# Kernel tuning notes

Measured on AMD Instinct MI355X. Metric: run time of the kernel, lower is better.

Reference implementation:

```python
import jax, jax.numpy as jnp
import numpy as np

NUM_NODES = 50000
NUM_EDGES = 640000
H_DIM = 128
OUT_DIM = 128
NUM_RELS = 16
NUM_BASES = 8


def _rgcn_layer(h, basis, coef, bias, src, dst, etype, norm, activation):
    # Basis decomposition: W[r] = sum_b coef[r,b] * basis[b]  -> [R, d_in, d_out]
    W = jnp.einsum('rb,bio->rio', coef, basis)
    # Transform node features under every relation: [R, N, d_out]
    Hr = jnp.einsum('ni,rio->rno', h, W)
    # Per-edge message: pick (relation, source) pair, apply edge norm. [E, d_out]
    msg = Hr[etype, src] * norm
    # Aggregate messages at destination nodes. [N, d_out]
    out = jax.ops.segment_sum(msg, dst, num_segments=h.shape[0])
    out = out + bias
    return activation(out) if activation is not None else out


def setup_inputs() -> dict:
    key = jax.random.key(0)
    ks = jax.random.split(key, 10)
    h = jax.random.normal(ks[0], (NUM_NODES, H_DIM), dtype=jnp.float32)
    norm = jax.random.uniform(ks[1], (NUM_EDGES, 1), dtype=jnp.float32)
    src = jax.random.randint(ks[2], (NUM_EDGES,), 0, NUM_NODES, dtype=jnp.int32)
    dst = jax.random.randint(ks[3], (NUM_EDGES,), 0, NUM_NODES, dtype=jnp.int32)
    etype = jax.random.randint(ks[4], (NUM_EDGES,), 0, NUM_RELS, dtype=jnp.int32)
    s1 = 1.0 / np.sqrt(H_DIM)
    s2 = 1.0 / np.sqrt(H_DIM)
    V1 = jax.random.normal(ks[5], (NUM_BASES, H_DIM, H_DIM), dtype=jnp.float32) * s1
    coef1 = jax.random.normal(ks[6], (NUM_RELS, NUM_BASES), dtype=jnp.float32) * (1.0 / np.sqrt(NUM_BASES))
    bias1 = jnp.zeros((H_DIM,), dtype=jnp.float32)
    V2 = jax.random.normal(ks[7], (NUM_BASES, H_DIM, OUT_DIM), dtype=jnp.float32) * s2
    coef2 = jax.random.normal(ks[8], (NUM_RELS, NUM_BASES), dtype=jnp.float32) * (1.0 / np.sqrt(NUM_BASES))
    bias2 = jnp.zeros((OUT_DIM,), dtype=jnp.float32)
    return {
        'h': h, 'norm': norm, 'src': src, 'dst': dst, 'etype': etype,
        'V1': V1, 'coef1': coef1, 'bias1': bias1,
        'V2': V2, 'coef2': coef2, 'bias2': bias2,
    }


def reference(h, norm, src, dst, etype, V1, coef1, bias1, V2, coef2, bias2):
    # Layer 0: relational graph conv with ReLU (hidden layer)
    h1 = _rgcn_layer(h, V1, coef1, bias1, src, dst, etype, norm, jax.nn.relu)
    # Layer 1+: BaseRGCN sorts edges by relation (bucketing for the low-mem
    # per-relation dispatch). The sort is a permutation of the edge set, so we
    # mirror it explicitly; the segment_sum result is mathematically identical.
    order = jnp.argsort(etype)
    src_s, dst_s, et_s, norm_s = src[order], dst[order], etype[order], norm[order]
    out = _rgcn_layer(h1, V2, coef2, bias2, src_s, dst_s, et_s, norm_s, None)
    return out
```

## Files before the change

### kernel.cpp

```cpp
#include <hip/hip_runtime.h>

#define N_RELS 16
#define N_BASES 8
#define HD 128
#define SCAN_B 1024
#define ROWS 32

typedef __attribute__((ext_vector_type(8))) short bf16x8;
typedef __attribute__((ext_vector_type(4))) float floatx4;
typedef __attribute__((ext_vector_type(2))) float floatx2;

__device__ __forceinline__ short bf16rn(float f) {
    union { float f; unsigned u; } v; v.f = f;
    unsigned u = v.u;
    unsigned r = (u + 0x7fffu + ((u >> 16) & 1u)) >> 16;
    return (short)r;
}

__device__ __forceinline__ unsigned packbf2(floatx2 a) {
    return ((unsigned)(unsigned short)bf16rn(a.y) << 16) | (unsigned short)bf16rn(a.x);
}


__global__ void setup_fused(const float* __restrict__ h, unsigned* __restrict__ hb, int n4,
                            const float* __restrict__ V1, const float* __restrict__ V2,
                            short* __restrict__ Vf,
                            const int* __restrict__ dst, int E, int* __restrict__ cnt,
                            int packBlocks, int vBlocks) {
    int blk = blockIdx.x;
    if (blk < packBlocks) {
        int i = blk * blockDim.x + threadIdx.x;
        if (i < n4) {
            float4 v = ((const float4*)h)[i];
            uint2 o;
            o.x = ((unsigned)(unsigned short)bf16rn(v.y) << 16) | (unsigned short)bf16rn(v.x);
            o.y = ((unsigned)(unsigned short)bf16rn(v.w) << 16) | (unsigned short)bf16rn(v.z);
            ((uint2*)hb)[i] = o;
        }
        return;
    }
    blk -= packBlocks;
    if (blk < vBlocks) {
        const float* V = ((blk & 8) ? V2 : V1) + (size_t)(blk & 7) * 16384;
        size_t obase = (size_t)blk * 16384;
        for (int e = threadIdx.x; e < 16384; e += blockDim.x) {
            float w = V[e];
            int k = e >> 7, n = e & 127;
            int kk = k >> 5, q = (k >> 3) & 3, j = k & 7;
            int lane = q * 16 + (n & 15);
            int idx = ((kk * 8 + (n >> 4)) * 64 + lane) * 8 + j;
            Vf[obase + idx] = bf16rn(w);
        }
        return;
    }
    blk -= vBlocks;
    int i = blk * blockDim.x + threadIdx.x;
    if (i < E) atomicAdd(&cnt[dst[i]], 1);
}


__global__ void scan_partial(const int* __restrict__ cnt, int N,
                             int* __restrict__ excl, int* __restrict__ bsum) {
    __shared__ int s[SCAN_B];
    int t = threadIdx.x, i = blockIdx.x * SCAN_B + t;
    int v = (i < N) ? cnt[i] : 0;
    s[t] = v; __syncthreads();
    for (int o = 1; o < SCAN_B; o <<= 1) {
        int x = (t >= o) ? s[t - o] : 0;
        __syncthreads();
        s[t] += x;
        __syncthreads();
    }
    if (i < N) excl[i] = s[t] - v;
    if (t == SCAN_B - 1) bsum[blockIdx.x] = s[t];
}

__global__ void scan_fixup(int* __restrict__ row_ptr, const int* __restrict__ bsum,
                           int nb, int N, int E, int* __restrict__ cursor) {
    __shared__ int pref[64];
    int t = threadIdx.x;
    if (t < 64) {
        int raw = (t < nb) ? bsum[t] : 0;
        int v = raw;
#pragma unroll
        for (int o = 1; o < 64; o <<= 1) {
            int u = __shfl_up(v, o, 64);
            if (t >= o) v += u;
        }
        pref[t] = v - raw;
    }
    __syncthreads();
    int i = blockIdx.x * blockDim.x + t;
    if (i < N) { int val = row_ptr[i] + pref[i >> 10]; row_ptr[i] = val; cursor[i] = val; }
    if (i == 0) row_ptr[N] = E;
}

__global__ void scatter_dst(const int* __restrict__ dst, const int* __restrict__ src,
                            const int* __restrict__ et, const float* __restrict__ norm,
                            int E, int* __restrict__ cursor, int2* __restrict__ edata) {
    int i = blockIdx.x * blockDim.x + threadIdx.x;
    if (i >= E) return;
    int p = atomicAdd(&cursor[dst[i]], 1);
    edata[p] = make_int2((et[i] << 16) | src[i], __float_as_int(norm[i]));
}


__global__ __launch_bounds__(512, 4) void rgcn_tile(
    const unsigned* __restrict__ hb, const int2* __restrict__ edata,
    const int* __restrict__ row_ptr, const float* __restrict__ coef,
    const short* __restrict__ Vf, const float* __restrict__ bias,
    void* __restrict__ outp, int N, int E, int mode) {
    __shared__ __align__(16) unsigned Zs[N_BASES][4][4][ROWS + 1][4];
    __shared__ __align__(16) float cofs[N_RELS * N_BASES];

    const int tid = threadIdx.x;
    const int wave = tid >> 6, lane = tid & 63;
    const int l16 = lane & 15;
    const int nb0 = blockIdx.x * ROWS;

    if (tid < N_RELS * N_BASES) cofs[tid] = coef[tid];
    __syncthreads();

    const int r = tid >> 4;
    const int node = nb0 + (r & 31);
    const int cn = (node < N) ? node : (N - 1);
    const int s = row_ptr[cn];
    const int t = row_ptr[cn + 1];
    const int len = (node < N) ? (t - s) : 0;

    int mx = len;
    mx = max(mx, __shfl_xor(mx, 16, 64));
    mx = max(mx, __shfl_xor(mx, 32, 64));
    const int nG = __builtin_amdgcn_readfirstlane(mx);

    floatx2 acc[4][N_BASES] = {};

    auto edix = [&](int j) { int ix = s + j; return (ix > E - 1) ? (E - 1) : ix; };
    auto gath = [&](int2 m) {
        return ((const uint4*)(hb + (size_t)(m.x & 0xffff) * 64))[l16];
    };
    auto procG = [&](int2 m, uint4 g, int j) {
        float nv = (j < len) ? __int_as_float(m.y) : 0.f;
        int ets = m.x >> 16;
        floatx4 c0 = *(const floatx4*)&cofs[ets * 8];
        floatx4 c1 = *(const floatx4*)&cofs[ets * 8 + 4];
        floatx2 v0, v1, v2, v3;
        v0.x = __uint_as_float(g.x << 16) * nv; v0.y = __uint_as_float(g.x & 0xffff0000u) * nv;
        v1.x = __uint_as_float(g.y << 16) * nv; v1.y = __uint_as_float(g.y & 0xffff0000u) * nv;
        v2.x = __uint_as_float(g.z << 16) * nv; v2.y = __uint_as_float(g.z & 0xffff0000u) * nv;
        v3.x = __uint_as_float(g.w << 16) * nv; v3.y = __uint_as_float(g.w & 0xffff0000u) * nv;
#pragma unroll
        for (int b = 0; b < N_BASES; b++) {
            float cw = (b < 4) ? c0[b & 3] : c1[b & 3];
            acc[0][b] = v0 * cw + acc[0][b];
            acc[1][b] = v1 * cw + acc[1][b];
            acc[2][b] = v2 * cw + acc[2][b];
            acc[3][b] = v3 * cw + acc[3][b];
        }
    };

    int2 m0 = edata[edix(0)];
    uint4 g0 = gath(m0);
    int2 m1 = edata[edix(1)];

    int k = 0;
    for (; k + 2 <= nG; k += 2) {
        uint4 g1 = gath(m1);
        procG(m0, g0, k);
        m0 = edata[edix(k + 2)];
        g0 = gath(m0);
        procG(m1, g1, k + 1);
        m1 = edata[edix(k + 3)];
    }
    if (k < nG) procG(m0, g0, k);

    {
        uint4 w;
#pragma unroll
        for (int b = 0; b < N_BASES; b++) {
            w.x = packbf2(acc[0][b]);
            w.y = packbf2(acc[1][b]);
            w.z = packbf2(acc[2][b]);
            w.w = packbf2(acc[3][b]);
            *(uint4*)&Zs[b][l16 >> 2][l16 & 3][r & 31][0] = w;
        }
    }
    __syncthreads();

    const int q = lane >> 4, cc = lane & 15;
    const int tt = wave;
    floatx4 ac0 = {}, ac1 = {};

#pragma unroll 2
    for (int b = 0; b < N_BASES; b++) {
#pragma unroll
        for (int kk = 0; kk < 4; kk++) {
            bf16x8 a0 = *(const bf16x8*)&Zs[b][kk][q][cc][0];
            bf16x8 a1 = *(const bf16x8*)&Zs[b][kk][q][16 + cc][0];
            bf16x8 B = *(const bf16x8*)(Vf + (size_t)b * 16384 +
                                        ((size_t)(kk * 8 + tt) * 64 + lane) * 8);
            ac0 = __builtin_amdgcn_mfma_f32_16x16x32_bf16(a0, B, ac0, 0, 0, 0);
            ac1 = __builtin_amdgcn_mfma_f32_16x16x32_bf16(a1, B, ac1, 0, 0, 0);
        }
    }

    float bv = bias[tt * 16 + cc];
    if (mode == 0) {
        unsigned short* o = (unsigned short*)outp;
#pragma unroll
        for (int mi = 0; mi < 2; mi++) {
            const floatx4& c = mi ? ac1 : ac0;
#pragma unroll
            for (int i = 0; i < 4; i++) {
                int nd = nb0 + mi * 16 + q * 4 + i;
                if (nd < N) {
                    float v = fmaxf(c[i] + bv, 0.f);
                    o[(size_t)nd * HD + tt * 16 + cc] = (unsigned short)bf16rn(v);
                }
            }
        }
    } else {
        float* o = (float*)outp;
#pragma unroll
        for (int mi = 0; mi < 2; mi++) {
            const floatx4& c = mi ? ac1 : ac0;
#pragma unroll
            for (int i = 0; i < 4; i++) {
                int nd = nb0 + mi * 16 + q * 4 + i;
                if (nd < N) o[(size_t)nd * HD + tt * 16 + cc] = c[i] + bv;
            }
        }
    }
}


extern "C" void kernel_launch(void* const* d_in, const int* in_sizes, int n_in,
                              void* d_out, int out_size, void* d_ws, size_t ws_size,
                              hipStream_t stream) {
    const float* h     = (const float*)d_in[0];
    const float* norm  = (const float*)d_in[1];
    const int*   src   = (const int*)d_in[2];
    const int*   dst   = (const int*)d_in[3];
    const int*   etype = (const int*)d_in[4];
    const float* V1    = (const float*)d_in[5];
    const float* coef1 = (const float*)d_in[6];
    const float* bias1 = (const float*)d_in[7];
    const float* V2    = (const float*)d_in[8];
    const float* coef2 = (const float*)d_in[9];
    const float* bias2 = (const float*)d_in[10];
    const int N = in_sizes[0] / HD;
    const int E = in_sizes[2];
    float* out = (float*)d_out;
    (void)n_in; (void)out_size; (void)ws_size;

    char* ws = (char*)d_ws;
    size_t off = 0;
    auto alloc = [&](size_t bytes) {
        void* p = ws + off;
        off += (bytes + 255) & ~(size_t)255;
        return p;
    };
    short*    Vf      = (short*)alloc((size_t)16 * 16384 * sizeof(short));
    unsigned* hb      = (unsigned*)alloc((size_t)N * 64 * sizeof(unsigned));
    unsigned* h1b     = (unsigned*)alloc((size_t)N * 64 * sizeof(unsigned));
    int2*     edata   = (int2*)alloc((size_t)E * sizeof(int2));
    int*      cnt     = (int*)alloc((size_t)N * sizeof(int));
    int*      row_ptr = (int*)alloc((size_t)(N + 1) * sizeof(int));
    int*      cursor  = (int*)alloc((size_t)N * sizeof(int));
    int*      bsum    = (int*)alloc(256 * sizeof(int));

    const int nb = (N + SCAN_B - 1) / SCAN_B;
    const int packBlocks = (N * 32 + 255) / 256;
    const int vBlocks = 16;
    const int histBlocks = (E + 255) / 256;

    hipMemsetAsync(cnt, 0, (size_t)N * sizeof(int), stream);
    setup_fused<<<packBlocks + vBlocks + histBlocks, 256, 0, stream>>>(
        h, hb, N * 32, V1, V2, Vf, dst, E, cnt, packBlocks, vBlocks);
    scan_partial<<<nb, SCAN_B, 0, stream>>>(cnt, N, row_ptr, bsum);
    scan_fixup<<<(N + 255) / 256, 256, 0, stream>>>(row_ptr, bsum, nb, N, E, cursor);
    scatter_dst<<<(E + 255) / 256, 256, 0, stream>>>(dst, src, etype, norm, E, cursor, edata);

    const int tiles = (N + ROWS - 1) / ROWS;

    rgcn_tile<<<tiles, 512, 0, stream>>>(hb, edata, row_ptr, coef1, Vf, bias1, h1b, N, E, 0);
    rgcn_tile<<<tiles, 512, 0, stream>>>(h1b, edata, row_ptr, coef2, Vf + (size_t)8 * 16384,
                                         bias2, out, N, E, 1);
}
```

Before: 304.6 us.

## Halve rows per block and spread each node's gather across 32 lanes

Each block now handles 16 destination nodes instead of 32. Each node gets 32 lanes that each load 4 bf16 features (uint2), where before 16 lanes each loaded 8. This halves per-thread accumulator registers and doubles the lanes per node, and the edge gather loop is deepened to a 3-way rotating pipeline unrolled by 6. The intent is more memory-level parallelism and occupancy for the irregular gather. In exchange it launches twice as many blocks, reloads the V basis per block for half as many rows, and wastes more iterations when nG is not a multiple of 6.

```diff
diff --git a/kernel.cpp b/kernel.cpp
--- a/kernel.cpp
+++ b/kernel.cpp
@@ -4,7 +4,7 @@
 #define N_BASES 8
 #define HD 128
 #define SCAN_B 1024
-#define ROWS 32
+#define ROWS 16
 
 typedef __attribute__((ext_vector_type(8))) short bf16x8;
 typedef __attribute__((ext_vector_type(4))) float floatx4;
@@ -115,92 +115,77 @@
 
     const int tid = threadIdx.x;
     const int wave = tid >> 6, lane = tid & 63;
-    const int l16 = lane & 15;
+    const int l32 = tid & 31;
     const int nb0 = blockIdx.x * ROWS;
 
     if (tid < N_RELS * N_BASES) cofs[tid] = coef[tid];
     __syncthreads();
 
-    const int r = tid >> 4;
-    const int node = nb0 + (r & 31);
+    const int r = tid >> 5;
+    const int node = nb0 + r;
     const int cn = (node < N) ? node : (N - 1);
     const int s = row_ptr[cn];
-    const int t = row_ptr[cn + 1];
-    const int len = (node < N) ? (t - s) : 0;
-
-    int mx = len;
-    mx = max(mx, __shfl_xor(mx, 16, 64));
-    mx = max(mx, __shfl_xor(mx, 32, 64));
+    const int len = (node < N) ? (row_ptr[cn + 1] - s) : 0;
+
+    int mx = max(len, __shfl_xor(len, 32, 64));
     const int nG = __builtin_amdgcn_readfirstlane(mx);
 
-    floatx2 acc[4][N_BASES] = {};
+    floatx2 a0[N_BASES] = {}, a1[N_BASES] = {};
+    const uint2* hbp = (const uint2*)hb;
 
     auto edix = [&](int j) { int ix = s + j; return (ix > E - 1) ? (E - 1) : ix; };
-    auto gath = [&](int2 m) {
-        return ((const uint4*)(hb + (size_t)(m.x & 0xffff) * 64))[l16];
-    };
-    auto procG = [&](int2 m, uint4 g, int j) {
+    auto gath = [&](int2 m) { return hbp[(size_t)(m.x & 0xffff) * 32 + l32]; };
+    auto proc = [&](int2 m, uint2 g, int j) {
         float nv = (j < len) ? __int_as_float(m.y) : 0.f;
         int ets = m.x >> 16;
         floatx4 c0 = *(const floatx4*)&cofs[ets * 8];
         floatx4 c1 = *(const floatx4*)&cofs[ets * 8 + 4];
-        floatx2 v0, v1, v2, v3;
+        floatx2 v0, v1;
         v0.x = __uint_as_float(g.x << 16) * nv; v0.y = __uint_as_float(g.x & 0xffff0000u) * nv;
         v1.x = __uint_as_float(g.y << 16) * nv; v1.y = __uint_as_float(g.y & 0xffff0000u) * nv;
-        v2.x = __uint_as_float(g.z << 16) * nv; v2.y = __uint_as_float(g.z & 0xffff0000u) * nv;
-        v3.x = __uint_as_float(g.w << 16) * nv; v3.y = __uint_as_float(g.w & 0xffff0000u) * nv;
 #pragma unroll
         for (int b = 0; b < N_BASES; b++) {
-            float cw = (b < 4) ? c0[b & 3] : c1[b & 3];
-            acc[0][b] = v0 * cw + acc[0][b];
-            acc[1][b] = v1 * cw + acc[1][b];
-            acc[2][b] = v2 * cw + acc[2][b];
-            acc[3][b] = v3 * cw + acc[3][b];
+            float cw = (b < 4) ? c0[b] : c1[b - 4];
+            a0[b] = v0 * cw + a0[b];
+            a1[b] = v1 * cw + a1[b];
         }
     };
 
-    int2 m0 = edata[edix(0)];
-    uint4 g0 = gath(m0);
-    int2 m1 = edata[edix(1)];
-
-    int k = 0;
-    for (; k + 2 <= nG; k += 2) {
-        uint4 g1 = gath(m1);
-        procG(m0, g0, k);
-        m0 = edata[edix(k + 2)];
-        g0 = gath(m0);
-        procG(m1, g1, k + 1);
-        m1 = edata[edix(k + 3)];
-    }
-    if (k < nG) procG(m0, g0, k);
+    int2 mA = edata[edix(0)], mB = edata[edix(1)], mC = edata[edix(2)];
+    uint2 gA = gath(mA), gB;
+
+    for (int k = 0; k < nG; k += 6) {
+        gB = gath(mB); proc(mA, gA, k);     mA = edata[edix(k + 3)];
+        gA = gath(mC); proc(mB, gB, k + 1); mB = edata[edix(k + 4)];
+        gB = gath(mA); proc(mC, gA, k + 2); mC = edata[edix(k + 5)];
+        gA = gath(mB); proc(mA, gB, k + 3); mA = edata[edix(k + 6)];
+        gB = gath(mC); proc(mB, gA, k + 4); mB = edata[edix(k + 7)];
+        gA = gath(mA); proc(mC, gB, k + 5); mC = edata[edix(k + 8)];
+    }
 
     {
-        uint4 w;
+        uint2 w;
 #pragma unroll
         for (int b = 0; b < N_BASES; b++) {
-            w.x = packbf2(acc[0][b]);
-            w.y = packbf2(acc[1][b]);
-            w.z = packbf2(acc[2][b]);
-            w.w = packbf2(acc[3][b]);
-            *(uint4*)&Zs[b][l16 >> 2][l16 & 3][r & 31][0] = w;
+            w.x = packbf2(a0[b]);
+            w.y = packbf2(a1[b]);
+            *(uint2*)&Zs[b][l32 >> 3][(l32 >> 1) & 3][r][(l32 & 1) * 2] = w;
         }
     }
     __syncthreads();
 
     const int q = lane >> 4, cc = lane & 15;
     const int tt = wave;
-    floatx4 ac0 = {}, ac1 = {};
+    floatx4 ac = {};
 
 #pragma unroll 2
     for (int b = 0; b < N_BASES; b++) {
 #pragma unroll
         for (int kk = 0; kk < 4; kk++) {
-            bf16x8 a0 = *(const bf16x8*)&Zs[b][kk][q][cc][0];
-            bf16x8 a1 = *(const bf16x8*)&Zs[b][kk][q][16 + cc][0];
+            bf16x8 a = *(const bf16x8*)&Zs[b][kk][q][cc][0];
             bf16x8 B = *(const bf16x8*)(Vf + (size_t)b * 16384 +
                                         ((size_t)(kk * 8 + tt) * 64 + lane) * 8);
-            ac0 = __builtin_amdgcn_mfma_f32_16x16x32_bf16(a0, B, ac0, 0, 0, 0);
-            ac1 = __builtin_amdgcn_mfma_f32_16x16x32_bf16(a1, B, ac1, 0, 0, 0);
+            ac = __builtin_amdgcn_mfma_f32_16x16x32_bf16(a, B, ac, 0, 0, 0);
         }
     }
 
@@ -208,27 +193,19 @@
     if (mode == 0) {
         unsigned short* o = (unsigned short*)outp;
 #pragma unroll
-        for (int mi = 0; mi < 2; mi++) {
-            const floatx4& c = mi ? ac1 : ac0;
-#pragma unroll
-            for (int i = 0; i < 4; i++) {
-                int nd = nb0 + mi * 16 + q * 4 + i;
-                if (nd < N) {
-                    float v = fmaxf(c[i] + bv, 0.f);
-                    o[(size_t)nd * HD + tt * 16 + cc] = (unsigned short)bf16rn(v);
-                }
+        for (int i = 0; i < 4; i++) {
+            int nd = nb0 + q * 4 + i;
+            if (nd < N) {
+                float v = fmaxf(ac[i] + bv, 0.f);
+                o[(size_t)nd * HD + tt * 16 + cc] = (unsigned short)bf16rn(v);
             }
         }
     } else {
         float* o = (float*)outp;
 #pragma unroll
-        for (int mi = 0; mi < 2; mi++) {
-            const floatx4& c = mi ? ac1 : ac0;
-#pragma unroll
-            for (int i = 0; i < 4; i++) {
-                int nd = nb0 + mi * 16 + q * 4 + i;
-                if (nd < N) o[(size_t)nd * HD + tt * 16 + cc] = c[i] + bv;
-            }
+        for (int i = 0; i < 4; i++) {
+            int nd = nb0 + q * 4 + i;
+            if (nd < N) o[(size_t)nd * HD + tt * 16 + cc] = ac[i] + bv;
         }
     }
 }
```

Result: slower. 355.5 us (+16.7%).

## Merge setup, histogram, scan and scatter into one cooperative kernel

Applied to the files above, without the earlier changes.

Replaces the memset and four preprocessing launches (pack/histogram, two scan passes, scatter) with a single cooperative kernel that uses grid-wide syncs between phases. The scan is redone as 64-element wave chunks with a single-wave pass over chunk sums. The goal is to remove launch overhead and inter-kernel gaps. In exchange it adds grid.sync barriers, fixes the grid at 1024 blocks, and serialises the chunk-sum scan on one wave, which could be slower than the separate kernels.

```diff
diff --git a/kernel.cpp b/kernel.cpp
--- a/kernel.cpp
+++ b/kernel.cpp
@@ -1,9 +1,11 @@
 #include <hip/hip_runtime.h>
+#include <hip/hip_cooperative_groups.h>
+
+namespace cg = cooperative_groups;
 
 #define N_RELS 16
 #define N_BASES 8
 #define HD 128
-#define SCAN_B 1024
 #define ROWS 32
 
 typedef __attribute__((ext_vector_type(8))) short bf16x8;
@@ -22,86 +24,93 @@
 }
 
 
-__global__ void setup_fused(const float* __restrict__ h, unsigned* __restrict__ hb, int n4,
-                            const float* __restrict__ V1, const float* __restrict__ V2,
-                            short* __restrict__ Vf,
-                            const int* __restrict__ dst, int E, int* __restrict__ cnt,
-                            int packBlocks, int vBlocks) {
-    int blk = blockIdx.x;
-    if (blk < packBlocks) {
-        int i = blk * blockDim.x + threadIdx.x;
-        if (i < n4) {
-            float4 v = ((const float4*)h)[i];
-            uint2 o;
-            o.x = ((unsigned)(unsigned short)bf16rn(v.y) << 16) | (unsigned short)bf16rn(v.x);
-            o.y = ((unsigned)(unsigned short)bf16rn(v.w) << 16) | (unsigned short)bf16rn(v.z);
-            ((uint2*)hb)[i] = o;
-        }
-        return;
-    }
-    blk -= packBlocks;
-    if (blk < vBlocks) {
+__global__ void setup_all(const float* __restrict__ h, unsigned* __restrict__ hb,
+                          const float* __restrict__ V1, const float* __restrict__ V2,
+                          short* __restrict__ Vf,
+                          const int* __restrict__ dst, const int* __restrict__ src,
+                          const int* __restrict__ et, const float* __restrict__ norm,
+                          int* __restrict__ cnt, int* __restrict__ row_ptr,
+                          int* __restrict__ cursor, int* __restrict__ bsum,
+                          int* __restrict__ bpre, int2* __restrict__ edata,
+                          int N, int E) {
+    cg::grid_group grid = cg::this_grid();
+    const int tid = threadIdx.x;
+    const int gid = blockIdx.x;
+    const int gtid = gid * blockDim.x + tid;
+    const int GSZ = gridDim.x * blockDim.x;
+    const int lane = tid & 63;
+    const int nchunk = (N + 63) >> 6;
+
+    for (int i = gtid; i < N; i += GSZ) cnt[i] = 0;
+    const int n4 = N * 32;
+    for (int i = gtid; i < n4; i += GSZ) {
+        float4 v = ((const float4*)h)[i];
+        uint2 o;
+        o.x = ((unsigned)(unsigned short)bf16rn(v.y) << 16) | (unsigned short)bf16rn(v.x);
+        o.y = ((unsigned)(unsigned short)bf16rn(v.w) << 16) | (unsigned short)bf16rn(v.z);
+        ((uint2*)hb)[i] = o;
+    }
+    for (int x = gtid; x < 16 * 16384; x += GSZ) {
+        int blk = x >> 14, e = x & 16383;
         const float* V = ((blk & 8) ? V2 : V1) + (size_t)(blk & 7) * 16384;
-        size_t obase = (size_t)blk * 16384;
-        for (int e = threadIdx.x; e < 16384; e += blockDim.x) {
-            float w = V[e];
-            int k = e >> 7, n = e & 127;
-            int kk = k >> 5, q = (k >> 3) & 3, j = k & 7;
-            int lane = q * 16 + (n & 15);
-            int idx = ((kk * 8 + (n >> 4)) * 64 + lane) * 8 + j;
-            Vf[obase + idx] = bf16rn(w);
-        }
-        return;
-    }
-    blk -= vBlocks;
-    int i = blk * blockDim.x + threadIdx.x;
-    if (i < E) atomicAdd(&cnt[dst[i]], 1);
-}
-
-
-__global__ void scan_partial(const int* __restrict__ cnt, int N,
-                             int* __restrict__ excl, int* __restrict__ bsum) {
-    __shared__ int s[SCAN_B];
-    int t = threadIdx.x, i = blockIdx.x * SCAN_B + t;
-    int v = (i < N) ? cnt[i] : 0;
-    s[t] = v; __syncthreads();
-    for (int o = 1; o < SCAN_B; o <<= 1) {
-        int x = (t >= o) ? s[t - o] : 0;
-        __syncthreads();
-        s[t] += x;
-        __syncthreads();
-    }
-    if (i < N) excl[i] = s[t] - v;
-    if (t == SCAN_B - 1) bsum[blockIdx.x] = s[t];
-}
-
-__global__ void scan_fixup(int* __restrict__ row_ptr, const int* __restrict__ bsum,
-                           int nb, int N, int E, int* __restrict__ cursor) {
-    __shared__ int pref[64];
-    int t = threadIdx.x;
-    if (t < 64) {
-        int raw = (t < nb) ? bsum[t] : 0;
-        int v = raw;
+        float w = V[e];
+        int k = e >> 7, n = e & 127;
+        int kk = k >> 5, q = (k >> 3) & 3, j = k & 7;
+        int ln = q * 16 + (n & 15);
+        int idx = ((kk * 8 + (n >> 4)) * 64 + ln) * 8 + j;
+        Vf[(size_t)blk * 16384 + idx] = bf16rn(w);
+    }
+    grid.sync();
+
+    for (int i = gtid; i < E; i += GSZ) atomicAdd(&cnt[dst[i]], 1);
+    grid.sync();
+
+    if (gid < nchunk && tid < 64) {
+        int i = gid * 64 + lane;
+        int v = (i < N) ? cnt[i] : 0;
+        int incl = v;
 #pragma unroll
         for (int o = 1; o < 64; o <<= 1) {
-            int u = __shfl_up(v, o, 64);
-            if (t >= o) v += u;
-        }
-        pref[t] = v - raw;
-    }
-    __syncthreads();
-    int i = blockIdx.x * blockDim.x + t;
-    if (i < N) { int val = row_ptr[i] + pref[i >> 10]; row_ptr[i] = val; cursor[i] = val; }
-    if (i == 0) row_ptr[N] = E;
-}
-
-__global__ void scatter_dst(const int* __restrict__ dst, const int* __restrict__ src,
-                            const int* __restrict__ et, const float* __restrict__ norm,
-                            int E, int* __restrict__ cursor, int2* __restrict__ edata) {
-    int i = blockIdx.x * blockDim.x + threadIdx.x;
-    if (i >= E) return;
-    int p = atomicAdd(&cursor[dst[i]], 1);
-    edata[p] = make_int2((et[i] << 16) | src[i], __float_as_int(norm[i]));
+            int u = __shfl_up(incl, o, 64);
+            if (lane >= o) incl += u;
+        }
+        if (i < N) row_ptr[i] = incl - v;
+        if (lane == 63) bsum[gid] = incl;
+    }
+    grid.sync();
+
+    if (gid == 0 && tid < 64) {
+        int carry = 0;
+        for (int c0 = 0; c0 < nchunk; c0 += 64) {
+            int c = c0 + lane;
+            int v = (c < nchunk) ? bsum[c] : 0;
+            int incl = v;
+#pragma unroll
+            for (int o = 1; o < 64; o <<= 1) {
+                int u = __shfl_up(incl, o, 64);
+                if (lane >= o) incl += u;
+            }
+            if (c < nchunk) bpre[c] = carry + incl - v;
+            carry += __shfl(incl, 63, 64);
+        }
+    }
+    grid.sync();
+
+    if (gid < nchunk && tid < 64) {
+        int i = gid * 64 + lane;
+        if (i < N) {
+            int val = row_ptr[i] + bpre[gid];
+            row_ptr[i] = val;
+            cursor[i] = val;
+        }
+    }
+    if (gtid == 0) row_ptr[N] = E;
+    grid.sync();
+
+    for (int i = gtid; i < E; i += GSZ) {
+        int p = atomicAdd(&cursor[dst[i]], 1);
+        edata[p] = make_int2((et[i] << 16) | src[i], __float_as_int(norm[i]));
+    }
 }
 
 
@@ -122,11 +131,10 @@
     __syncthreads();
 
     const int r = tid >> 4;
-    const int node = nb0 + (r & 31);
+    const int node = nb0 + r;
     const int cn = (node < N) ? node : (N - 1);
     const int s = row_ptr[cn];
-    const int t = row_ptr[cn + 1];
-    const int len = (node < N) ? (t - s) : 0;
+    const int len = (node < N) ? (row_ptr[cn + 1] - s) : 0;
 
     int mx = len;
     mx = max(mx, __shfl_xor(mx, 16, 64));
@@ -182,7 +190,7 @@
             w.y = packbf2(acc[1][b]);
             w.z = packbf2(acc[2][b]);
             w.w = packbf2(acc[3][b]);
-            *(uint4*)&Zs[b][l16 >> 2][l16 & 3][r & 31][0] = w;
+            *(uint4*)&Zs[b][l16 >> 2][l16 & 3][r][0] = w;
         }
     }
     __syncthreads();
@@ -195,12 +203,12 @@
     for (int b = 0; b < N_BASES; b++) {
 #pragma unroll
         for (int kk = 0; kk < 4; kk++) {
-            bf16x8 a0 = *(const bf16x8*)&Zs[b][kk][q][cc][0];
-            bf16x8 a1 = *(const bf16x8*)&Zs[b][kk][q][16 + cc][0];
+            bf16x8 a = *(const bf16x8*)&Zs[b][kk][q][cc][0];
+            bf16x8 am = *(const bf16x8*)&Zs[b][kk][q][16 + cc][0];
             bf16x8 B = *(const bf16x8*)(Vf + (size_t)b * 16384 +
                                         ((size_t)(kk * 8 + tt) * 64 + lane) * 8);
-            ac0 = __builtin_amdgcn_mfma_f32_16x16x32_bf16(a0, B, ac0, 0, 0, 0);
-            ac1 = __builtin_amdgcn_mfma_f32_16x16x32_bf16(a1, B, ac1, 0, 0, 0);
+            ac0 = __builtin_amdgcn_mfma_f32_16x16x32_bf16(a, B, ac0, 0, 0, 0);
+            ac1 = __builtin_amdgcn_mfma_f32_16x16x32_bf16(am, B, ac1, 0, 0, 0);
         }
     }
 
@@ -267,19 +275,19 @@
     int*      cnt     = (int*)alloc((size_t)N * sizeof(int));
     int*      row_ptr = (int*)alloc((size_t)(N + 1) * sizeof(int));
     int*      cursor  = (int*)alloc((size_t)N * sizeof(int));
-    int*      bsum    = (int*)alloc(256 * sizeof(int));
-
-    const int nb = (N + SCAN_B - 1) / SCAN_B;
-    const int packBlocks = (N * 32 + 255) / 256;
-    const int vBlocks = 16;
-    const int histBlocks = (E + 255) / 256;
-
-    hipMemsetAsync(cnt, 0, (size_t)N * sizeof(int), stream);
-    setup_fused<<<packBlocks + vBlocks + histBlocks, 256, 0, stream>>>(
-        h, hb, N * 32, V1, V2, Vf, dst, E, cnt, packBlocks, vBlocks);
-    scan_partial<<<nb, SCAN_B, 0, stream>>>(cnt, N, row_ptr, bsum);
-    scan_fixup<<<(N + 255) / 256, 256, 0, stream>>>(row_ptr, bsum, nb, N, E, cursor);
-    scatter_dst<<<(E + 255) / 256, 256, 0, stream>>>(dst, src, etype, norm, E, cursor, edata);
+    int*      bsum    = (int*)alloc(1024 * sizeof(int));
+    int*      bpre    = (int*)alloc(1024 * sizeof(int));
+
+    {
+        void* args[] = {
+            (void*)&h, (void*)&hb, (void*)&V1, (void*)&V2, (void*)&Vf,
+            (void*)&dst, (void*)&src, (void*)&etype, (void*)&norm,
+            (void*)&cnt, (void*)&row_ptr, (void*)&cursor, (void*)&bsum,
+            (void*)&bpre, (void*)&edata, (void*)&N, (void*)&E
+        };
+        hipLaunchCooperativeKernel((void*)setup_all, dim3(1024), dim3(256),
+                                   args, 0, stream);
+    }
 
     const int tiles = (N + ROWS - 1) / ROWS;
 
```

Measured after the change: 815.8 us. 2.68x slower.
